# Kernel optimization log

Measured on AMD Instinct MI355X. Metric: run time of the kernel, lower is better.

The kernel has to match this reference:

```python
import jax, jax.numpy as jnp
import numpy as np
from jax.scipy.special import ndtri
from jax.scipy.stats import norm

B, C, S = 8192, 1024, 16  # batch, num_classes, sample_size


def setup_inputs() -> dict:
    key = jax.random.key(0)
    k1, k2 = jax.random.split(key)
    logits = jax.random.normal(k1, (B, C), dtype=jnp.float32)
    labels = jax.random.randint(k2, (B,), 0, C, dtype=jnp.int32)
    temperature = jnp.ones((1,), dtype=jnp.float32)
    return {"logits": logits, "labels": labels, "temperature": temperature}


def _exact_loss(logits, labels, temperature, sample_size=S):
    # Global batch-norm of logits (torch .std() is unbiased -> ddof=1).
    logits = (logits - logits.mean()) / jnp.std(logits, ddof=1)
    num_classes = logits.shape[-1]
    # logits_deltas: target logit minus every logit, target column excluded via mask.
    tgt = jnp.take_along_axis(logits, labels[:, None], axis=-1)  # (B, 1)
    delta = (tgt - logits) / temperature[0]                      # (B, C)
    alt_mask = 1.0 - jax.nn.one_hot(labels, num_classes, dtype=logits.dtype)  # 0 at target
    # PositiveNormalProb: P(delta_j + eps_y - eps_j > 0 for all j != y),
    # eps iid N(0,1). Conditioning on eps_y = t gives independent events:
    #   prob = E_{t~N(0,1)}[ prod_j Phi(delta_j + t) ]
    # integrated with sample_size midpoint quantile nodes t_k = Phi^{-1}((k+0.5)/S).
    grid = (jnp.arange(sample_size, dtype=logits.dtype) + 0.5) / sample_size
    t = ndtri(grid)                                              # (S,)
    logcdf = norm.logcdf(delta[:, None, :] + t[None, :, None])   # (B, S, C)
    logp = jnp.sum(logcdf * alt_mask[:, None, :], axis=-1)       # (B, S)
    probs = jnp.mean(jnp.exp(logp), axis=-1)                     # (B,)
    # reduction = 'mean': expected error rate
    return 1.0 - probs.mean()


def reference(logits, labels, temperature):
    return _exact_loss(logits, labels, temperature)
```

## Files before the change

### kernel.cpp

```cpp
#include <hip/hip_runtime.h>
#include <math.h>

#define NB 8192
#define NC 1024
#define NS 16

#define NT   2464
#define NTR  2461
#define C0   48
#define BMAXF 1984.0f
#define UBIAS 978.5f

constexpr int OFFK[16] = {0, 69, 109, 139, 164, 187, 208, 228,
                          248, 268, 289, 312, 337, 367, 407, 476};

#define TICKET 2
#define PSUM  16
#define PSQ   1040
#define RCNT  2064
#define RLIST 3088
#define PART  11280
#define TAB   11408
#define NBLK_MAIN 128

__device__ __forceinline__ float log_ndtr_f(float x) {
    float e = erfcf(-x * 0.70710678118654752f);
    if (e > 1e-37f) return __logf(0.5f * e);
    return -0.5f * x * x - 0.91893853320467274f - __logf(-x);
}

__global__ __launch_bounds__(256) void k_pre(const float* __restrict__ logits,
                                             const int* __restrict__ labels,
                                             float* __restrict__ ws) {
    const int bid = blockIdx.x;
    if (bid >= 1024) {
        if (bid == 1024 && threadIdx.x == 0) ((int*)ws)[TICKET] = 0;
        int i = (bid - 1024) * 256 + threadIdx.x;
        if (i < NT) {
            int ii = i < NTR ? i : (NTR - 1);
            float x = -9.5f + (float)ii * (1.0f / 128.0f);
            ws[TAB + i] = log_ndtr_f(x);
        }
        return;
    }
    const int w = threadIdx.x >> 6, l = threadIdx.x & 63;
    const float4* lf4 = (const float4*)logits;
    __shared__ int flags[8];
    __shared__ float bs[4], bss[4];
    float s = 0.0f, ss = 0.0f;
    for (int rr = 0; rr < 2; ++rr) {
        const int row = bid * 8 + w * 2 + rr;
        const float tgt = logits[row * NC + labels[row]];
        int cnt = 0;
        #pragma unroll
        for (int i = 0; i < 4; ++i) {
            float4 v = lf4[row * (NC / 4) + l + 64 * i];
            s  += v.x + v.y + v.z + v.w;
            ss += v.x * v.x + v.y * v.y + v.z * v.z + v.w * v.w;
            cnt += (v.x >= tgt) + (v.y >= tgt) + (v.z >= tgt) + (v.w >= tgt);
        }
        #pragma unroll
        for (int m = 32; m; m >>= 1) cnt += __shfl_xor(cnt, m, 64);
        if (l == 0) flags[w * 2 + rr] = ((cnt - 1) < C0);
    }
    #pragma unroll
    for (int m = 32; m; m >>= 1) {
        s  += __shfl_xor(s,  m, 64);
        ss += __shfl_xor(ss, m, 64);
    }
    if (l == 0) { bs[w] = s; bss[w] = ss; }
    __syncthreads();
    if (threadIdx.x == 0) {
        ws[PSUM + bid] = bs[0] + bs[1] + bs[2] + bs[3];
        ws[PSQ + bid]  = bss[0] + bss[1] + bss[2] + bss[3];
        int* wsi = (int*)ws;
        int n = 0;
        #pragma unroll
        for (int i = 0; i < 8; ++i)
            if (flags[i]) wsi[RLIST + bid * 8 + (n++)] = bid * 8 + i;
        wsi[RCNT + bid] = n;
    }
}

__global__ __launch_bounds__(256) void k_main(const float* __restrict__ logits,
                                              const int* __restrict__ labels,
                                              const float* __restrict__ temp,
                                              float* __restrict__ ws,
                                              float* __restrict__ out) {
    const int bid = blockIdx.x, tid = threadIdx.x;
    const int* wsi = (const int*)ws;
    const int w = tid >> 6, l = tid & 63;

    __shared__ float lt[NT];
    __shared__ int   P[1024];
    __shared__ int   wtot[4];
    __shared__ float rs[4], rss[4];
    __shared__ float shInv;
    __shared__ float wprob[4];
    __shared__ int   shLast;

    float4* lt4 = (float4*)lt;
    const float4* gt4 = (const float4*)(ws + TAB);
    for (int i = tid; i < NT / 4; i += 256) lt4[i] = gt4[i];

    int c4[4];
    const int b4 = tid * 4;
    #pragma unroll
    for (int j = 0; j < 4; ++j) c4[j] = wsi[RCNT + b4 + j];
    int s4 = c4[0] + c4[1] + c4[2] + c4[3];
    int v = s4;
    #pragma unroll
    for (int off = 1; off < 64; off <<= 1) {
        int u = __shfl_up(v, off, 64);
        if (l >= off) v += u;
    }
    if (l == 63) wtot[w] = v;

    float s  = ws[PSUM + tid] + ws[PSUM + 256 + tid] + ws[PSUM + 512 + tid] + ws[PSUM + 768 + tid];
    float ss = ws[PSQ + tid]  + ws[PSQ + 256 + tid]  + ws[PSQ + 512 + tid]  + ws[PSQ + 768 + tid];
    #pragma unroll
    for (int m = 32; m; m >>= 1) {
        s  += __shfl_xor(s,  m, 64);
        ss += __shfl_xor(ss, m, 64);
    }
    if (l == 0) { rs[w] = s; rss[w] = ss; }
    __syncthreads();

    int wbase = 0;
    #pragma unroll
    for (int ww = 0; ww < 4; ++ww) if (ww < w) wbase += wtot[ww];
    int ex = wbase + v - s4;
    P[b4 + 0] = ex;
    P[b4 + 1] = ex + c4[0];
    P[b4 + 2] = ex + c4[0] + c4[1];
    P[b4 + 3] = ex + c4[0] + c4[1] + c4[2];
    const int Ntot = wtot[0] + wtot[1] + wtot[2] + wtot[3];

    if (tid == 0) {
        float S1 = rs[0] + rs[1] + rs[2] + rs[3];
        float S2 = rss[0] + rss[1] + rss[2] + rss[3];
        const float N = (float)NB * (float)NC;
        float var = (S2 - S1 * S1 / N) / (N - 1.0f);
        shInv = 128.0f / (sqrtf(var) * temp[0]);
    }
    __syncthreads();
    const float s128 = shInv;

    const float4* lf4 = (const float4*)logits;
    float waveProb = 0.0f;
    const int gwave = bid * 4 + w;

    for (int i = gwave; i < Ntot; i += NBLK_MAIN * 4) {
        int lo = 0, hi = 1023;
        while (lo < hi) {
            int mid = (lo + hi + 1) >> 1;
            if (P[mid] <= i) lo = mid; else hi = mid - 1;
        }
        const int row = wsi[RLIST + lo * 8 + (i - P[lo])];

        const float tgt = logits[row * NC + labels[row]];
        const float A = fmaf(tgt, s128, UBIAS);
        float a[16];
        #pragma unroll
        for (int k = 0; k < 16; ++k) a[k] = 0.0f;
        #pragma unroll
        for (int ii = 0; ii < 4; ++ii) {
            float4 vv4 = lf4[row * (NC / 4) + l + 64 * ii];
            float vv[4] = {vv4.x, vv4.y, vv4.z, vv4.w};
            #pragma unroll
            for (int j = 0; j < 4; ++j) {
                float u = fmaf(vv[j], -s128, A);
                u = fminf(fmaxf(u, 0.0f), BMAXF);
                int bi = (int)u;
                #pragma unroll
                for (int k = 0; k < 16; ++k) a[k] += lt[bi + OFFK[k]];
            }
        }
        #pragma unroll
        for (int k = 0; k < 16; ++k) {
            #pragma unroll
            for (int m = 32; m; m >>= 1) a[k] += __shfl_xor(a[k], m, 64);
        }
        float uy = fmaf(tgt, -s128, A);
        uy = fminf(fmaxf(uy, 0.0f), BMAXF);
        int by = (int)uy;
        float prob = 0.0f;
        #pragma unroll
        for (int k = 0; k < 16; ++k) prob += __expf(a[k] - lt[by + OFFK[k]]);
        waveProb += prob * (1.0f / 16.0f);
    }

    if (l == 0) wprob[w] = waveProb;
    __syncthreads();

    if (tid == 0) {
        float part = wprob[0] + wprob[1] + wprob[2] + wprob[3];
        __hip_atomic_store(&ws[PART + bid], part, __ATOMIC_RELAXED,
                           __HIP_MEMORY_SCOPE_AGENT);
        int t = __hip_atomic_fetch_add((int*)ws + TICKET, 1, __ATOMIC_ACQ_REL,
                                       __HIP_MEMORY_SCOPE_AGENT);
        shLast = (t == NBLK_MAIN - 1);
    }
    __syncthreads();
    if (shLast) {
        float p = 0.0f;
        if (tid < NBLK_MAIN)
            p = __hip_atomic_load(&ws[PART + tid], __ATOMIC_RELAXED,
                                  __HIP_MEMORY_SCOPE_AGENT);
        #pragma unroll
        for (int m = 32; m; m >>= 1) p += __shfl_xor(p, m, 64);
        if (l == 0) wprob[w] = p;
        __syncthreads();
        if (tid == 0)
            out[0] = 1.0f - (wprob[0] + wprob[1]) * (1.0f / (float)NB);
    }
}

extern "C" void kernel_launch(void* const* d_in, const int* in_sizes, int n_in,
                              void* d_out, int out_size, void* d_ws, size_t ws_size,
                              hipStream_t stream) {
    const float* logits = (const float*)d_in[0];
    const int*   labels = (const int*)d_in[1];
    const float* temp   = (const float*)d_in[2];
    float* ws  = (float*)d_ws;
    float* out = (float*)d_out;

    hipLaunchKernelGGL(k_pre,  dim3(1024 + (NT + 255) / 256), dim3(256), 0, stream,
                       logits, labels, ws);
    hipLaunchKernelGGL(k_main, dim3(NBLK_MAIN), dim3(256), 0, stream,
                       logits, labels, temp, ws, out);
}
```

Baseline: 21.49 us.

## Compact candidate rows as bitmasks, build table in-block, widen main kernel

The pre-pass now stores per-block 8-bit candidate masks and target logits instead of per-block row lists, and it no longer builds the log-CDF lookup table. The main kernel builds that table itself in shared memory and uses 512 threads per block. Each wave decodes its row from a popcount prefix scan plus bit scanning, and the target logit comes from the stored copy instead of a labels gather. The goal is to cut extra pre-pass blocks, scattered reads, and scan work, at the cost of redundant table computation in every main block.

```diff
diff --git a/kernel.cpp b/kernel.cpp
--- a/kernel.cpp
+++ b/kernel.cpp
@@ -3,7 +3,6 @@
 
 #define NB 8192
 #define NC 1024
-#define NS 16
 
 #define NT   2464
 #define NTR  2461
@@ -14,13 +13,12 @@
 constexpr int OFFK[16] = {0, 69, 109, 139, 164, 187, 208, 228,
                           248, 268, 289, 312, 337, 367, 407, 476};
 
-#define TICKET 2
-#define PSUM  16
-#define PSQ   1040
-#define RCNT  2064
-#define RLIST 3088
-#define PART  11280
-#define TAB   11408
+#define TICKET 3
+#define PSUM   16
+#define PSQ    1040
+#define RTGT   2064
+#define RMASKF 10256
+#define PART   10512
 #define NBLK_MAIN 128
 
 __device__ __forceinline__ float log_ndtr_f(float x) {
@@ -33,171 +31,186 @@
                                              const int* __restrict__ labels,
                                              float* __restrict__ ws) {
     const int bid = blockIdx.x;
-    if (bid >= 1024) {
-        if (bid == 1024 && threadIdx.x == 0) ((int*)ws)[TICKET] = 0;
-        int i = (bid - 1024) * 256 + threadIdx.x;
-        if (i < NT) {
-            int ii = i < NTR ? i : (NTR - 1);
-            float x = -9.5f + (float)ii * (1.0f / 128.0f);
-            ws[TAB + i] = log_ndtr_f(x);
-        }
-        return;
-    }
     const int w = threadIdx.x >> 6, l = threadIdx.x & 63;
+    if (bid == 0 && threadIdx.x == 0) ((int*)ws)[TICKET] = 0;
+
+    __shared__ int   flags[8];
+    __shared__ float tgts[8];
+    __shared__ float bs[4], bss[4];
+
     const float4* lf4 = (const float4*)logits;
-    __shared__ int flags[8];
-    __shared__ float bs[4], bss[4];
+    const int row0 = bid * 8 + w * 2;
+    const int lab0 = labels[row0], lab1 = labels[row0 + 1];
+    const float tgt0 = logits[row0 * NC + lab0];
+    const float tgt1 = logits[(row0 + 1) * NC + lab1];
+
     float s = 0.0f, ss = 0.0f;
-    for (int rr = 0; rr < 2; ++rr) {
-        const int row = bid * 8 + w * 2 + rr;
-        const float tgt = logits[row * NC + labels[row]];
-        int cnt = 0;
-        #pragma unroll
-        for (int i = 0; i < 4; ++i) {
-            float4 v = lf4[row * (NC / 4) + l + 64 * i];
-            s  += v.x + v.y + v.z + v.w;
-            ss += v.x * v.x + v.y * v.y + v.z * v.z + v.w * v.w;
-            cnt += (v.x >= tgt) + (v.y >= tgt) + (v.z >= tgt) + (v.w >= tgt);
-        }
-        #pragma unroll
-        for (int m = 32; m; m >>= 1) cnt += __shfl_xor(cnt, m, 64);
-        if (l == 0) flags[w * 2 + rr] = ((cnt - 1) < C0);
+    int c0 = 0, c1 = 0;
+    #pragma unroll
+    for (int i = 0; i < 4; ++i) {
+        float4 v = lf4[row0 * (NC / 4) + l + 64 * i];
+        s  += v.x + v.y + v.z + v.w;
+        ss += v.x * v.x + v.y * v.y + v.z * v.z + v.w * v.w;
+        c0 += (v.x >= tgt0) + (v.y >= tgt0) + (v.z >= tgt0) + (v.w >= tgt0);
+    }
+    #pragma unroll
+    for (int i = 0; i < 4; ++i) {
+        float4 v = lf4[(row0 + 1) * (NC / 4) + l + 64 * i];
+        s  += v.x + v.y + v.z + v.w;
+        ss += v.x * v.x + v.y * v.y + v.z * v.z + v.w * v.w;
+        c1 += (v.x >= tgt1) + (v.y >= tgt1) + (v.z >= tgt1) + (v.w >= tgt1);
     }
     #pragma unroll
     for (int m = 32; m; m >>= 1) {
+        c0 += __shfl_xor(c0, m, 64);
+        c1 += __shfl_xor(c1, m, 64);
         s  += __shfl_xor(s,  m, 64);
         ss += __shfl_xor(ss, m, 64);
     }
-    if (l == 0) { bs[w] = s; bss[w] = ss; }
-    __syncthreads();
+    if (l == 0) {
+        flags[w * 2 + 0] = ((c0 - 1) < C0);
+        flags[w * 2 + 1] = ((c1 - 1) < C0);
+        tgts[w * 2 + 0] = tgt0;
+        tgts[w * 2 + 1] = tgt1;
+        bs[w] = s; bss[w] = ss;
+    }
+    __syncthreads();
+    if (threadIdx.x < 8) ws[RTGT + bid * 8 + threadIdx.x] = tgts[threadIdx.x];
     if (threadIdx.x == 0) {
         ws[PSUM + bid] = bs[0] + bs[1] + bs[2] + bs[3];
         ws[PSQ + bid]  = bss[0] + bss[1] + bss[2] + bss[3];
-        int* wsi = (int*)ws;
-        int n = 0;
-        #pragma unroll
-        for (int i = 0; i < 8; ++i)
-            if (flags[i]) wsi[RLIST + bid * 8 + (n++)] = bid * 8 + i;
-        wsi[RCNT + bid] = n;
-    }
-}
-
-__global__ __launch_bounds__(256) void k_main(const float* __restrict__ logits,
-                                              const int* __restrict__ labels,
+        unsigned char m = 0;
+        #pragma unroll
+        for (int i = 0; i < 8; ++i) m |= (unsigned char)(flags[i] << i);
+        ((unsigned char*)(ws + RMASKF))[bid] = m;
+    }
+}
+
+__global__ __launch_bounds__(512) void k_main(const float* __restrict__ logits,
                                               const float* __restrict__ temp,
                                               float* __restrict__ ws,
                                               float* __restrict__ out) {
     const int bid = blockIdx.x, tid = threadIdx.x;
-    const int* wsi = (const int*)ws;
     const int w = tid >> 6, l = tid & 63;
+    int* wsi = (int*)ws;
 
     __shared__ float lt[NT];
-    __shared__ int   P[1024];
+    __shared__ int   M[256], P[256];
     __shared__ int   wtot[4];
-    __shared__ float rs[4], rss[4];
+    __shared__ float bs[8], bss[8];
     __shared__ float shInv;
-    __shared__ float wprob[4];
-    __shared__ int   shLast;
-
-    float4* lt4 = (float4*)lt;
-    const float4* gt4 = (const float4*)(ws + TAB);
-    for (int i = tid; i < NT / 4; i += 256) lt4[i] = gt4[i];
-
-    int c4[4];
-    const int b4 = tid * 4;
-    #pragma unroll
-    for (int j = 0; j < 4; ++j) c4[j] = wsi[RCNT + b4 + j];
-    int s4 = c4[0] + c4[1] + c4[2] + c4[3];
-    int v = s4;
-    #pragma unroll
-    for (int off = 1; off < 64; off <<= 1) {
-        int u = __shfl_up(v, off, 64);
-        if (l >= off) v += u;
-    }
-    if (l == 63) wtot[w] = v;
-
-    float s  = ws[PSUM + tid] + ws[PSUM + 256 + tid] + ws[PSUM + 512 + tid] + ws[PSUM + 768 + tid];
-    float ss = ws[PSQ + tid]  + ws[PSQ + 256 + tid]  + ws[PSQ + 512 + tid]  + ws[PSQ + 768 + tid];
+    __shared__ float wacc[8];
+    __shared__ int   shNtot, shLast;
+
+    int m4 = 0, cpc = 0, v = 0;
+    if (tid < 256) { m4 = wsi[RMASKF + tid]; M[tid] = m4; }
+    float s  = ws[PSUM + tid] + ws[PSUM + 512 + tid];
+    float ss = ws[PSQ + tid]  + ws[PSQ + 512 + tid];
+
+    for (int i = tid; i < NT; i += 512) {
+        int ii = i < NTR ? i : (NTR - 1);
+        lt[i] = log_ndtr_f(-9.5f + (float)ii * (1.0f / 128.0f));
+    }
+
+    if (tid < 256) {
+        cpc = __popc(m4);
+        v = cpc;
+        #pragma unroll
+        for (int off = 1; off < 64; off <<= 1) {
+            int u = __shfl_up(v, off, 64);
+            if (l >= off) v += u;
+        }
+        if (l == 63) wtot[w] = v;
+    }
     #pragma unroll
     for (int m = 32; m; m >>= 1) {
         s  += __shfl_xor(s,  m, 64);
         ss += __shfl_xor(ss, m, 64);
     }
-    if (l == 0) { rs[w] = s; rss[w] = ss; }
-    __syncthreads();
-
-    int wbase = 0;
-    #pragma unroll
-    for (int ww = 0; ww < 4; ++ww) if (ww < w) wbase += wtot[ww];
-    int ex = wbase + v - s4;
-    P[b4 + 0] = ex;
-    P[b4 + 1] = ex + c4[0];
-    P[b4 + 2] = ex + c4[0] + c4[1];
-    P[b4 + 3] = ex + c4[0] + c4[1] + c4[2];
-    const int Ntot = wtot[0] + wtot[1] + wtot[2] + wtot[3];
-
+    if (l == 0) { bs[w] = s; bss[w] = ss; }
+    __syncthreads();
+
+    if (tid < 256) {
+        int wb = 0;
+        #pragma unroll
+        for (int ww = 0; ww < 4; ++ww) if (ww < w) wb += wtot[ww];
+        P[tid] = wb + v - cpc;
+    }
     if (tid == 0) {
-        float S1 = rs[0] + rs[1] + rs[2] + rs[3];
-        float S2 = rss[0] + rss[1] + rss[2] + rss[3];
+        shNtot = wtot[0] + wtot[1] + wtot[2] + wtot[3];
+        float S1 = 0.0f, S2 = 0.0f;
+        #pragma unroll
+        for (int i = 0; i < 8; ++i) { S1 += bs[i]; S2 += bss[i]; }
         const float N = (float)NB * (float)NC;
         float var = (S2 - S1 * S1 / N) / (N - 1.0f);
         shInv = 128.0f / (sqrtf(var) * temp[0]);
     }
     __syncthreads();
+
+    const int Ntot = shNtot;
     const float s128 = shInv;
-
     const float4* lf4 = (const float4*)logits;
-    float waveProb = 0.0f;
-    const int gwave = bid * 4 + w;
-
-    for (int i = gwave; i < Ntot; i += NBLK_MAIN * 4) {
-        int lo = 0, hi = 1023;
-        while (lo < hi) {
-            int mid = (lo + hi + 1) >> 1;
-            if (P[mid] <= i) lo = mid; else hi = mid - 1;
+    float waveAcc = 0.0f;
+
+    if (bid * 8 < Ntot) {
+        const int g = bid * 8 + w;
+        for (int i = g; i < Ntot; i += NBLK_MAIN * 8) {
+            int lo = 0, hi = 255;
+            #pragma unroll
+            for (int st = 0; st < 8; ++st) {
+                int mid = (lo + hi + 1) >> 1;
+                if (P[mid] <= i) lo = mid; else hi = mid - 1;
+            }
+            int idx = i - P[lo];
+            int mm = M[lo];
+            for (int t = 0; t < idx; ++t) mm &= mm - 1;
+            const int row = lo * 32 + (__ffs(mm) - 1);
+
+            const float tgt = ws[RTGT + row];
+            const float A = fmaf(tgt, s128, UBIAS);
+            float a[16];
+            #pragma unroll
+            for (int k = 0; k < 16; ++k) a[k] = 0.0f;
+            #pragma unroll
+            for (int ii = 0; ii < 4; ++ii) {
+                float4 vv4 = lf4[row * (NC / 4) + l + 64 * ii];
+                float vv[4] = {vv4.x, vv4.y, vv4.z, vv4.w};
+                #pragma unroll
+                for (int j = 0; j < 4; ++j) {
+                    float u = fmaf(vv[j], -s128, A);
+                    u = fminf(fmaxf(u, 0.0f), BMAXF);
+                    int bi = (int)u;
+                    #pragma unroll
+                    for (int k = 0; k < 16; ++k) a[k] += lt[bi + OFFK[k]];
+                }
+            }
+            #pragma unroll
+            for (int k = 0; k < 16; ++k) {
+                #pragma unroll
+                for (int m = 32; m; m >>= 1) a[k] += __shfl_xor(a[k], m, 64);
+            }
+            if (l == 0) {
+                float uy = fmaf(tgt, -s128, A);
+                uy = fminf(fmaxf(uy, 0.0f), BMAXF);
+                int by = (int)uy;
+                float prob = 0.0f;
+                #pragma unroll
+                for (int k = 0; k < 16; ++k) prob += __expf(a[k] - lt[by + OFFK[k]]);
+                waveAcc += prob * (1.0f / 16.0f);
+            }
         }
-        const int row = wsi[RLIST + lo * 8 + (i - P[lo])];
-
-        const float tgt = logits[row * NC + labels[row]];
-        const float A = fmaf(tgt, s128, UBIAS);
-        float a[16];
-        #pragma unroll
-        for (int k = 0; k < 16; ++k) a[k] = 0.0f;
-        #pragma unroll
-        for (int ii = 0; ii < 4; ++ii) {
-            float4 vv4 = lf4[row * (NC / 4) + l + 64 * ii];
-            float vv[4] = {vv4.x, vv4.y, vv4.z, vv4.w};
-            #pragma unroll
-            for (int j = 0; j < 4; ++j) {
-                float u = fmaf(vv[j], -s128, A);
-                u = fminf(fmaxf(u, 0.0f), BMAXF);
-                int bi = (int)u;
-                #pragma unroll
-                for (int k = 0; k < 16; ++k) a[k] += lt[bi + OFFK[k]];
-            }
-        }
-        #pragma unroll
-        for (int k = 0; k < 16; ++k) {
-            #pragma unroll
-            for (int m = 32; m; m >>= 1) a[k] += __shfl_xor(a[k], m, 64);
-        }
-        float uy = fmaf(tgt, -s128, A);
-        uy = fminf(fmaxf(uy, 0.0f), BMAXF);
-        int by = (int)uy;
-        float prob = 0.0f;
-        #pragma unroll
-        for (int k = 0; k < 16; ++k) prob += __expf(a[k] - lt[by + OFFK[k]]);
-        waveProb += prob * (1.0f / 16.0f);
-    }
-
-    if (l == 0) wprob[w] = waveProb;
+    }
+
+    if (l == 0) wacc[w] = waveAcc;
     __syncthreads();
 
     if (tid == 0) {
-        float part = wprob[0] + wprob[1] + wprob[2] + wprob[3];
+        float part = 0.0f;
+        #pragma unroll
+        for (int i = 0; i < 8; ++i) part += wacc[i];
         __hip_atomic_store(&ws[PART + bid], part, __ATOMIC_RELAXED,
                            __HIP_MEMORY_SCOPE_AGENT);
-        int t = __hip_atomic_fetch_add((int*)ws + TICKET, 1, __ATOMIC_ACQ_REL,
+        int t = __hip_atomic_fetch_add(wsi + TICKET, 1, __ATOMIC_ACQ_REL,
                                        __HIP_MEMORY_SCOPE_AGENT);
         shLast = (t == NBLK_MAIN - 1);
     }
@@ -209,10 +222,14 @@
                                   __HIP_MEMORY_SCOPE_AGENT);
         #pragma unroll
         for (int m = 32; m; m >>= 1) p += __shfl_xor(p, m, 64);
-        if (l == 0) wprob[w] = p;
+        if (l == 0) wacc[w] = p; else if (tid >= NBLK_MAIN && l == 0) wacc[w] = 0.0f;
         __syncthreads();
-        if (tid == 0)
-            out[0] = 1.0f - (wprob[0] + wprob[1]) * (1.0f / (float)NB);
+        if (tid == 0) {
+            float tot = 0.0f;
+            #pragma unroll
+            for (int i = 0; i < 8; ++i) tot += wacc[i];
+            out[0] = 1.0f - tot * (1.0f / (float)NB);
+        }
     }
 }
 
@@ -225,8 +242,8 @@
     float* ws  = (float*)d_ws;
     float* out = (float*)d_out;
 
-    hipLaunchKernelGGL(k_pre,  dim3(1024 + (NT + 255) / 256), dim3(256), 0, stream,
+    hipLaunchKernelGGL(k_pre,  dim3(1024),      dim3(256), 0, stream,
                        logits, labels, ws);
-    hipLaunchKernelGGL(k_main, dim3(NBLK_MAIN), dim3(256), 0, stream,
-                       logits, labels, temp, ws, out);
-}
+    hipLaunchKernelGGL(k_main, dim3(NBLK_MAIN), dim3(512), 0, stream,
+                       logits, temp, ws, out);
+}
```

New measurement: 24.12 us. 12.2% more time.
